# Performance work log

Measured on AMD Instinct MI355X. Metric: run time of the kernel, lower is better.

Reference implementation:

```python
import jax, jax.numpy as jnp
import numpy as np

B = 4
IN_DIM = 512
HID = 1024
MLP_LAYERS = 2
SEQ = 4096          # output_dim / sequence_length
RH = 64             # ripl_hidden_dim
RL = 2              # ripl_num_layers
MULT = 1            # ripl_coordinate_multipler

MID_DIM = 2 * RH * RH + (RH + 1) * RH      # per middle ripple layer param count
OUT_DIM = 2 * RH * 1 + (RH + 1) * 1        # output ripple layer param count
MLP_OUT = RL * MID_DIM + OUT_DIM


def gelu(x):
    return jax.nn.gelu(x, approximate=False)


def layer_norm(x, g, b, eps=1e-5):
    mu = jnp.mean(x, axis=-1, keepdims=True)
    var = jnp.var(x, axis=-1, keepdims=True)
    return (x - mu) * jax.lax.rsqrt(var + eps) * g + b


def batch_ripple(x, w, b):
    # x: (B,S,I), w: (B,O,I,2), b: (B,O,I+1)
    # out[b,s,o] = b[b,o,0] + sum_i b[b,o,i+1] * sin(w[b,o,i,0]*x[b,s,i] + w[b,o,i,1])
    arg = w[:, None, :, :, 0] * x[:, :, None, :] + w[:, None, :, :, 1]  # (B,S,O,I)
    return b[:, None, :, 0] + jnp.sum(jnp.sin(arg) * b[:, None, :, 1:], axis=-1)


def setup_inputs() -> dict:
    key = jax.random.key(0)
    ks = jax.random.split(key, 20)
    s = 0.02
    inp = {
        "x": jax.random.normal(ks[0], (B, IN_DIM), jnp.float32),
        "mlp_w0": jax.random.normal(ks[1], (IN_DIM, HID), jnp.float32) * s,
        "mlp_b0": jnp.zeros((HID,), jnp.float32),
        "mlp_w1": jax.random.normal(ks[2], (HID, HID), jnp.float32) * s,
        "mlp_b1": jnp.zeros((HID,), jnp.float32),
        "ln_g1": jnp.ones((HID,), jnp.float32),
        "ln_b1": jnp.zeros((HID,), jnp.float32),
        "mlp_w2": jax.random.normal(ks[3], (HID, HID), jnp.float32) * s,
        "mlp_b2": jnp.zeros((HID,), jnp.float32),
        "ln_g2": jnp.ones((HID,), jnp.float32),
        "ln_b2": jnp.zeros((HID,), jnp.float32),
        "mlp_w3": jax.random.normal(ks[4], (HID, MLP_OUT), jnp.float32) * s,
        "mlp_b3": jnp.zeros((MLP_OUT,), jnp.float32),
        "lc_w": jax.random.normal(ks[5], (1, RH), jnp.float32) * 0.1,
        "lc_b": jax.random.normal(ks[6], (RH,), jnp.float32) * 0.1,
        "byp_w": jax.random.normal(ks[7], (1, 1, 2), jnp.float32),
        "byp_b": jax.random.normal(ks[8], (1, 2), jnp.float32),
    }
    return inp


def reference(x, mlp_w0, mlp_b0, mlp_w1, mlp_b1, ln_g1, ln_b1,
              mlp_w2, mlp_b2, ln_g2, ln_b2, mlp_w3, mlp_b3,
              lc_w, lc_b, byp_w, byp_b):
    # hypernetwork MLP: Linear+GELU, [Linear+LN+GELU]*2, Linear
    h = gelu(x @ mlp_w0 + mlp_b0)
    h = gelu(layer_norm(h @ mlp_w1 + mlp_b1, ln_g1, ln_b1))
    h = gelu(layer_norm(h @ mlp_w2 + mlp_b2, ln_g2, ln_b2))
    mlp_out = h @ mlp_w3 + mlp_b3                      # (B, MLP_OUT)

    # split into RL middle ripple layers then the output layer
    middles = [mlp_out[:, i * MID_DIM:(i + 1) * MID_DIM] for i in range(RL)]
    out_w = mlp_out[:, RL * MID_DIM:RL * MID_DIM + OUT_DIM]

    # line coordinates -> fc layer
    lc = (jnp.arange(SEQ, dtype=jnp.float32) * MULT)[None, :, None]  # (1,S,1)
    lc = jnp.broadcast_to(lc, (x.shape[0], SEQ, 1))
    lc_x = lc @ lc_w + lc_b                                          # (B,S,RH)
    lc_bypass = lc_x

    for mw in middles:
        w = mw[:, :2 * RH * RH].reshape(-1, RH, RH, 2)
        b = mw[:, 2 * RH * RH:].reshape(-1, RH, RH + 1)
        lc_x = gelu(batch_ripple(lc_x, w, b))

    wo = out_w[:, :2 * RH].reshape(-1, 1, RH, 2)
    bo = out_w[:, 2 * RH:].reshape(-1, 1, RH + 1)
    lc_x = batch_ripple(lc_x, wo, bo)                                # (B,S,1)

    # learned RippleLinear(1,1) bypass, broadcast over features then reduced
    byp = byp_b[0, 0] + jnp.sum(
        jnp.sin(byp_w[0, 0, 0] * lc_bypass + byp_w[0, 0, 1]) * byp_b[0, 1],
        axis=-1, keepdims=True)
    lc_x = lc_x + byp
    return jnp.transpose(lc_x, (0, 2, 1))                            # (B,1,S)
```

## Files before the change

### kernel.cpp

```cpp
#include <hip/hip_runtime.h>
#include <math.h>

#define B_      4
#define IN_DIM  512
#define HID     1024
#define SEQ     4096
#define MID_DIM 12352
#define MLP_OUT 24897
#define INV2PI  0.15915494309189535f

#define MLPT_STRIDE 25088

#define OFF_P0    0
#define OFF_P1    32768
#define OFF_P2    49152
#define OFF_MLPT  65536

__device__ __forceinline__ float gelu_exact(float v) {
    return 0.5f * v * (1.0f + erff(v * 0.70710678118654752f));
}

__device__ __forceinline__ float hw_sin_rev(float r) {
    r = r - __builtin_rintf(r);
    return __builtin_amdgcn_sinf(r);
}

__global__ void k_gemm0(const float* __restrict__ x, const float* __restrict__ w0,
                        float* __restrict__ p0) {
    const int cch = blockIdx.x, kc = blockIdx.y;
    const int tid = threadIdx.x;
    __shared__ float xs[256];
    {
        const int b = tid >> 6, k = tid & 63;
        xs[tid] = x[b * IN_DIM + kc * 64 + k];
    }
    __syncthreads();
    const int b = tid >> 6, cl = tid & 63;
    const int c = cch * 64 + cl;
    const float* wp = w0 + (size_t)(kc * 64) * HID + c;
    const float* xp = xs + b * 64;
    float acc = 0.f;
    #pragma unroll 16
    for (int k = 0; k < 64; ++k) acc = fmaf(xp[k], wp[(size_t)k * HID], acc);
    p0[(kc * 4 + b) * HID + c] = acc;
}

__global__ void k_gemm1(const float* __restrict__ p0, const float* __restrict__ b0,
                        const float* __restrict__ w1, float* __restrict__ p1) {
    const int cch = blockIdx.x, kc = blockIdx.y;
    const int tid = threadIdx.x;
    __shared__ float s_h[1024];
    for (int e = tid; e < 1024; e += 256) {
        const int b = e >> 8, kk = e & 255;
        const int kg = kc * 256 + kk;
        float v = b0[kg];
        #pragma unroll
        for (int j = 0; j < 8; ++j) v += p0[(j * 4 + b) * HID + kg];
        s_h[e] = gelu_exact(v);
    }
    __syncthreads();
    const int b = tid >> 6, cl = tid & 63;
    const int c = cch * 64 + cl;
    const float* wp = w1 + (size_t)(kc * 256) * HID + c;
    const float* hp = s_h + b * 256;
    float acc = 0.f;
    #pragma unroll 16
    for (int k = 0; k < 256; ++k) acc = fmaf(hp[k], wp[(size_t)k * HID], acc);
    p1[(kc * 4 + b) * HID + c] = acc;
}

__global__ void k_gemm2(const float* __restrict__ p1, const float* __restrict__ b1,
                        const float* __restrict__ g1, const float* __restrict__ bl1,
                        const float* __restrict__ w2, float* __restrict__ p2) {
    const int cch = blockIdx.x, kc = blockIdx.y;
    const int tid = threadIdx.x;
    __shared__ __align__(16) float vbuf[4096];
    __shared__ float s_h[1024];
    __shared__ float s_red[8];
    for (int e = tid; e < 4096; e += 256) {
        const int b = e >> 10, c = e & 1023;
        float v = b1[c];
        #pragma unroll
        for (int j = 0; j < 4; ++j) v += p1[(j * 4 + b) * HID + c];
        vbuf[e] = v;
    }
    __syncthreads();
    {
        const int b = tid >> 6, lane = tid & 63;
        float s1 = 0.f, s2 = 0.f;
        #pragma unroll
        for (int jj = 0; jj < 16; ++jj) {
            const float v = vbuf[b * 1024 + lane + 64 * jj];
            s1 += v; s2 += v * v;
        }
        #pragma unroll
        for (int m = 1; m < 64; m <<= 1) {
            s1 += __shfl_xor(s1, m, 64);
            s2 += __shfl_xor(s2, m, 64);
        }
        if (lane == 0) {
            const float mu = s1 * (1.0f / HID);
            s_red[b] = mu;
            s_red[4 + b] = rsqrtf(s2 * (1.0f / HID) - mu * mu + 1e-5f);
        }
    }
    __syncthreads();
    for (int e = tid; e < 1024; e += 256) {
        const int b = e >> 8, kk = e & 255;
        const int c = kc * 256 + kk;
        const float v = vbuf[b * 1024 + c];
        s_h[e] = gelu_exact((v - s_red[b]) * s_red[4 + b] * g1[c] + bl1[c]);
    }
    __syncthreads();
    const int b = tid >> 6, cl = tid & 63;
    const int c = cch * 64 + cl;
    const float* wp = w2 + (size_t)(kc * 256) * HID + c;
    const float* hp = s_h + b * 256;
    float acc = 0.f;
    #pragma unroll 16
    for (int k = 0; k < 256; ++k) acc = fmaf(hp[k], wp[(size_t)k * HID], acc);
    p2[(kc * 4 + b) * HID + c] = acc;
}

__global__ void k_gemm3T(const float* __restrict__ p2, const float* __restrict__ b2,
                         const float* __restrict__ g2, const float* __restrict__ bl2,
                         const float* __restrict__ w3, const float* __restrict__ b3,
                         float* __restrict__ mlpT) {
    const int colb = blockIdx.x;
    const int kc   = blockIdx.y;
    const int tid  = threadIdx.x;
    __shared__ __align__(16) float vbuf[4096];
    __shared__ __align__(16) float s_h[512];
    __shared__ float s_red[8];

    for (int e = tid; e < 4096; e += 256) {
        const int b = e >> 10, c = e & 1023;
        float v = b2[c];
        #pragma unroll
        for (int j = 0; j < 4; ++j) v += p2[(j * 4 + b) * HID + c];
        vbuf[e] = v;
    }
    __syncthreads();
    {
        const int b = tid >> 6, lane = tid & 63;
        float s1 = 0.f, s2 = 0.f;
        #pragma unroll
        for (int jj = 0; jj < 16; ++jj) {
            const float v = vbuf[b * 1024 + lane + 64 * jj];
            s1 += v; s2 += v * v;
        }
        #pragma unroll
        for (int m = 1; m < 64; m <<= 1) {
            s1 += __shfl_xor(s1, m, 64);
            s2 += __shfl_xor(s2, m, 64);
        }
        if (lane == 0) {
            const float mu = s1 * (1.0f / HID);
            s_red[b] = mu;
            s_red[4 + b] = rsqrtf(s2 * (1.0f / HID) - mu * mu + 1e-5f);
        }
    }
    __syncthreads();
    for (int e = tid; e < 512; e += 256) {
        const int b = e >> 7, kk = e & 127;
        const int c = kc * 128 + kk;
        const float v = vbuf[b * 1024 + c];
        s_h[e] = gelu_exact((v - s_red[b]) * s_red[4 + b] * g2[c] + bl2[c]);
    }
    __syncthreads();

    const int c_raw = colb * 256 + tid;
    const bool valid = c_raw < MLP_OUT;
    const int c = valid ? c_raw : (MLP_OUT - 1);
    const float* wp = w3 + (size_t)(kc * 128) * MLP_OUT + c;
    float a0 = 0.f, a1 = 0.f, a2 = 0.f, a3 = 0.f;
    #pragma unroll 8
    for (int kk = 0; kk < 128; kk += 4) {
        const float wv0 = wp[(size_t)(kk + 0) * MLP_OUT];
        const float wv1 = wp[(size_t)(kk + 1) * MLP_OUT];
        const float wv2 = wp[(size_t)(kk + 2) * MLP_OUT];
        const float wv3 = wp[(size_t)(kk + 3) * MLP_OUT];
        const float4 h0 = *reinterpret_cast<const float4*>(&s_h[kk]);
        const float4 h1 = *reinterpret_cast<const float4*>(&s_h[128 + kk]);
        const float4 h2 = *reinterpret_cast<const float4*>(&s_h[256 + kk]);
        const float4 h3 = *reinterpret_cast<const float4*>(&s_h[384 + kk]);
        a0 = fmaf(h0.x, wv0, fmaf(h0.y, wv1, fmaf(h0.z, wv2, fmaf(h0.w, wv3, a0))));
        a1 = fmaf(h1.x, wv0, fmaf(h1.y, wv1, fmaf(h1.z, wv2, fmaf(h1.w, wv3, a1))));
        a2 = fmaf(h2.x, wv0, fmaf(h2.y, wv1, fmaf(h2.z, wv2, fmaf(h2.w, wv3, a2))));
        a3 = fmaf(h3.x, wv0, fmaf(h3.y, wv1, fmaf(h3.z, wv2, fmaf(h3.w, wv3, a3))));
    }
    if (!valid) return;

    int d; float sc = 1.f;
    if (c < 2 * MID_DIM) {
        const int l = c / MID_DIM;
        const int rel = c - l * MID_DIM;
        if (rel < 8192) {
            const int o = rel >> 7, low = rel & 127;
            d = l * 12416 + (low & 1) * 4096 + (low >> 1) * 64 + o;
            sc = INV2PI;
        } else {
            const int r2 = rel - 8192;
            const int o = r2 / 65, j = r2 % 65;
            d = (j == 0) ? (l * 12416 + 12288 + o)
                         : (l * 12416 + 8192 + (j - 1) * 64 + o);
        }
    } else {
        const int rel = c - 2 * MID_DIM;
        if (rel < 128)       { d = 24832 + (rel & 1) * 64 + (rel >> 1); sc = INV2PI; }
        else if (rel == 128) { d = 24832 + 192; }
        else                 { d = 24832 + 128 + (rel - 129); }
    }
    const float bias = (kc == 0) ? b3[c] : 0.f;
    atomicAdd(&mlpT[(size_t)0 * MLPT_STRIDE + d], (a0 + bias) * sc);
    atomicAdd(&mlpT[(size_t)1 * MLPT_STRIDE + d], (a1 + bias) * sc);
    atomicAdd(&mlpT[(size_t)2 * MLPT_STRIDE + d], (a2 + bias) * sc);
    atomicAdd(&mlpT[(size_t)3 * MLPT_STRIDE + d], (a3 + bias) * sc);
}

__global__ void __launch_bounds__(256, 2) k_ripple(
        const float* __restrict__ mlpT, const float* __restrict__ lcw,
        const float* __restrict__ lcb, const float* __restrict__ bypw,
        const float* __restrict__ bypb, float* __restrict__ out) {
    const int tid = threadIdx.x;
    const int b = blockIdx.y;
    const int t0 = blockIdx.x * 32;
    const int lane = tid & 63, wid = tid >> 6, tb = wid * 8;

    __shared__ __align__(16) float s_w[12416];
    __shared__ __align__(16) float s_x[2304];
    __shared__ __align__(16) float s_wo[256];
    __shared__ float s_red[32];

    const float* mb = mlpT + (size_t)b * MLPT_STRIDE;

    {
        const float4* src = reinterpret_cast<const float4*>(mb);
        float4* dst = reinterpret_cast<float4*>(s_w);
        for (int e = tid; e < 3104; e += 256) dst[e] = src[e];
        if (tid < 64)
            reinterpret_cast<float4*>(s_wo)[tid] =
                reinterpret_cast<const float4*>(mb + 24832)[tid];
    }
    const float lw = lcw[lane], lb = lcb[lane];
    for (int e = tid; e < 2048; e += 256) {
        const int i = e >> 5, tt = e & 31;
        s_x[i * 36 + tt] = fmaf((float)(t0 + tt), lcw[i], lcb[i]);
    }
    __syncthreads();

    float acc[8];
    for (int layer = 0; layer < 2; ++layer) {
        const float bc = s_w[12288 + lane];
        #pragma unroll
        for (int j = 0; j < 8; ++j) acc[j] = bc;
        for (int i = 0; i < 64; ++i) {
            const float wsv = s_w[i * 64 + lane];
            const float wov = s_w[4096 + i * 64 + lane];
            const float bsv = s_w[8192 + i * 64 + lane];
            const float4 xa = *reinterpret_cast<const float4*>(&s_x[i * 36 + tb]);
            const float4 xb = *reinterpret_cast<const float4*>(&s_x[i * 36 + tb + 4]);
            const float xv[8] = {xa.x, xa.y, xa.z, xa.w, xb.x, xb.y, xb.z, xb.w};
            #pragma unroll
            for (int j = 0; j < 8; ++j) {
                const float r = fmaf(wsv, xv[j], wov);
                acc[j] = fmaf(hw_sin_rev(r), bsv, acc[j]);
            }
        }
        __syncthreads();
        if (layer == 0) {
            #pragma unroll
            for (int j = 0; j < 8; ++j)
                s_x[lane * 36 + tb + j] = gelu_exact(acc[j]);
            const float4* src = reinterpret_cast<const float4*>(mb + 12416);
            float4* dst = reinterpret_cast<float4*>(s_w);
            for (int e = tid; e < 3104; e += 256) dst[e] = src[e];
            __syncthreads();
        }
    }

    {
        const float wsO = s_wo[lane], woO = s_wo[64 + lane], bsO = s_wo[128 + lane];
        const float bcO = s_wo[192];
        const float bw0 = bypw[0] * INV2PI, bw1 = bypw[1] * INV2PI;
        const float bb0 = bypb[0], bb1 = bypb[1];
        #pragma unroll
        for (int j = 0; j < 8; ++j) {
            const int t = t0 + tb + j;
            const float v = gelu_exact(acc[j]);
            float s = hw_sin_rev(fmaf(wsO, v, woO)) * bsO;
            const float xb = fmaf((float)t, lw, lb);
            s = fmaf(hw_sin_rev(fmaf(bw0, xb, bw1)), bb1, s);
            #pragma unroll
            for (int m = 1; m < 64; m <<= 1) s += __shfl_xor(s, m, 64);
            if (lane == 0) s_red[tb + j] = s + bcO + bb0;
        }
    }
    __syncthreads();
    if (tid < 32) out[(size_t)b * SEQ + t0 + tid] = s_red[tid];
}

extern "C" void kernel_launch(void* const* d_in, const int* in_sizes, int n_in,
                              void* d_out, int out_size, void* d_ws, size_t ws_size,
                              hipStream_t stream) {
    const float* x    = (const float*)d_in[0];
    const float* w0   = (const float*)d_in[1];
    const float* b0   = (const float*)d_in[2];
    const float* w1   = (const float*)d_in[3];
    const float* b1   = (const float*)d_in[4];
    const float* g1   = (const float*)d_in[5];
    const float* bl1  = (const float*)d_in[6];
    const float* w2   = (const float*)d_in[7];
    const float* b2   = (const float*)d_in[8];
    const float* g2   = (const float*)d_in[9];
    const float* bl2  = (const float*)d_in[10];
    const float* w3   = (const float*)d_in[11];
    const float* b3   = (const float*)d_in[12];
    const float* lcw  = (const float*)d_in[13];
    const float* lcb  = (const float*)d_in[14];
    const float* bypw = (const float*)d_in[15];
    const float* bypb = (const float*)d_in[16];
    float* out = (float*)d_out;
    float* ws  = (float*)d_ws;

    float* p0   = ws + OFF_P0;
    float* p1   = ws + OFF_P1;
    float* p2   = ws + OFF_P2;
    float* mlpT = ws + OFF_MLPT;

    k_gemm0 <<<dim3(16, 8), 256, 0, stream>>>(x, w0, p0);
    k_gemm1 <<<dim3(16, 4), 256, 0, stream>>>(p0, b0, w1, p1);
    k_gemm2 <<<dim3(16, 4), 256, 0, stream>>>(p1, b1, g1, bl1, w2, p2);
    hipMemsetAsync(mlpT, 0, (size_t)B_ * MLPT_STRIDE * sizeof(float), stream);
    k_gemm3T<<<dim3(98, 8), 256, 0, stream>>>(p2, b2, g2, bl2, w3, b3, mlpT);
    k_ripple<<<dim3(SEQ / 32, B_), 256, 0, stream>>>(mlpT, lcw, lcb, bypw, bypb, out);
}
```

Baseline: 310.1 us.

## Replace gemm3 atomics with partial buffer plus combine kernel, split K finer

The last MLP GEMM now writes per-K-chunk partial sums to a workspace buffer, and a new combine kernel reduces them, adds the bias and scatters into the transposed parameter layout. This replaces the memset and the atomicAdd scatter. The weight loads in gemm3 are software-pipelined with a 16-deep register double buffer, and gemm1/gemm2 double their K-split to run more blocks. The sine wrapper uses a fract builtin when available. In exchange it adds one kernel launch and extra partial-sum traffic through global memory.

```diff
diff --git a/kernel.cpp b/kernel.cpp
--- a/kernel.cpp
+++ b/kernel.cpp
@@ -13,16 +13,21 @@
 
 #define OFF_P0    0
 #define OFF_P1    32768
-#define OFF_P2    49152
-#define OFF_MLPT  65536
+#define OFF_P2    65536
+#define OFF_P3    98304
+#define OFF_MLPT  895008
 
 __device__ __forceinline__ float gelu_exact(float v) {
     return 0.5f * v * (1.0f + erff(v * 0.70710678118654752f));
 }
 
 __device__ __forceinline__ float hw_sin_rev(float r) {
+#if __has_builtin(__builtin_amdgcn_fractf)
+    return __builtin_amdgcn_sinf(__builtin_amdgcn_fractf(r));
+#else
     r = r - __builtin_rintf(r);
     return __builtin_amdgcn_sinf(r);
+#endif
 }
 
 __global__ void k_gemm0(const float* __restrict__ x, const float* __restrict__ w0,
@@ -49,10 +54,10 @@
                         const float* __restrict__ w1, float* __restrict__ p1) {
     const int cch = blockIdx.x, kc = blockIdx.y;
     const int tid = threadIdx.x;
-    __shared__ float s_h[1024];
-    for (int e = tid; e < 1024; e += 256) {
-        const int b = e >> 8, kk = e & 255;
-        const int kg = kc * 256 + kk;
+    __shared__ float s_h[512];
+    for (int e = tid; e < 512; e += 256) {
+        const int b = e >> 7, kk = e & 127;
+        const int kg = kc * 128 + kk;
         float v = b0[kg];
         #pragma unroll
         for (int j = 0; j < 8; ++j) v += p0[(j * 4 + b) * HID + kg];
@@ -61,11 +66,11 @@
     __syncthreads();
     const int b = tid >> 6, cl = tid & 63;
     const int c = cch * 64 + cl;
-    const float* wp = w1 + (size_t)(kc * 256) * HID + c;
-    const float* hp = s_h + b * 256;
+    const float* wp = w1 + (size_t)(kc * 128) * HID + c;
+    const float* hp = s_h + b * 128;
     float acc = 0.f;
     #pragma unroll 16
-    for (int k = 0; k < 256; ++k) acc = fmaf(hp[k], wp[(size_t)k * HID], acc);
+    for (int k = 0; k < 128; ++k) acc = fmaf(hp[k], wp[(size_t)k * HID], acc);
     p1[(kc * 4 + b) * HID + c] = acc;
 }
 
@@ -75,13 +80,13 @@
     const int cch = blockIdx.x, kc = blockIdx.y;
     const int tid = threadIdx.x;
     __shared__ __align__(16) float vbuf[4096];
-    __shared__ float s_h[1024];
+    __shared__ float s_h[512];
     __shared__ float s_red[8];
     for (int e = tid; e < 4096; e += 256) {
         const int b = e >> 10, c = e & 1023;
         float v = b1[c];
         #pragma unroll
-        for (int j = 0; j < 4; ++j) v += p1[(j * 4 + b) * HID + c];
+        for (int j = 0; j < 8; ++j) v += p1[(j * 4 + b) * HID + c];
         vbuf[e] = v;
     }
     __syncthreads();
@@ -105,39 +110,38 @@
         }
     }
     __syncthreads();
-    for (int e = tid; e < 1024; e += 256) {
-        const int b = e >> 8, kk = e & 255;
-        const int c = kc * 256 + kk;
+    for (int e = tid; e < 512; e += 256) {
+        const int b = e >> 7, kk = e & 127;
+        const int c = kc * 128 + kk;
         const float v = vbuf[b * 1024 + c];
         s_h[e] = gelu_exact((v - s_red[b]) * s_red[4 + b] * g1[c] + bl1[c]);
     }
     __syncthreads();
     const int b = tid >> 6, cl = tid & 63;
     const int c = cch * 64 + cl;
-    const float* wp = w2 + (size_t)(kc * 256) * HID + c;
-    const float* hp = s_h + b * 256;
+    const float* wp = w2 + (size_t)(kc * 128) * HID + c;
+    const float* hp = s_h + b * 128;
     float acc = 0.f;
     #pragma unroll 16
-    for (int k = 0; k < 256; ++k) acc = fmaf(hp[k], wp[(size_t)k * HID], acc);
+    for (int k = 0; k < 128; ++k) acc = fmaf(hp[k], wp[(size_t)k * HID], acc);
     p2[(kc * 4 + b) * HID + c] = acc;
 }
 
-__global__ void k_gemm3T(const float* __restrict__ p2, const float* __restrict__ b2,
-                         const float* __restrict__ g2, const float* __restrict__ bl2,
-                         const float* __restrict__ w3, const float* __restrict__ b3,
-                         float* __restrict__ mlpT) {
+__global__ void k_gemm3(const float* __restrict__ p2, const float* __restrict__ b2,
+                        const float* __restrict__ g2, const float* __restrict__ bl2,
+                        const float* __restrict__ w3, float* __restrict__ p3) {
     const int colb = blockIdx.x;
     const int kc   = blockIdx.y;
     const int tid  = threadIdx.x;
     __shared__ __align__(16) float vbuf[4096];
-    __shared__ __align__(16) float s_h[512];
+    __shared__ float s_h[512];
     __shared__ float s_red[8];
 
     for (int e = tid; e < 4096; e += 256) {
         const int b = e >> 10, c = e & 1023;
         float v = b2[c];
         #pragma unroll
-        for (int j = 0; j < 4; ++j) v += p2[(j * 4 + b) * HID + c];
+        for (int j = 0; j < 8; ++j) v += p2[(j * 4 + b) * HID + c];
         vbuf[e] = v;
     }
     __syncthreads();
@@ -173,24 +177,51 @@
     const bool valid = c_raw < MLP_OUT;
     const int c = valid ? c_raw : (MLP_OUT - 1);
     const float* wp = w3 + (size_t)(kc * 128) * MLP_OUT + c;
+
     float a0 = 0.f, a1 = 0.f, a2 = 0.f, a3 = 0.f;
-    #pragma unroll 8
-    for (int kk = 0; kk < 128; kk += 4) {
-        const float wv0 = wp[(size_t)(kk + 0) * MLP_OUT];
-        const float wv1 = wp[(size_t)(kk + 1) * MLP_OUT];
-        const float wv2 = wp[(size_t)(kk + 2) * MLP_OUT];
-        const float wv3 = wp[(size_t)(kk + 3) * MLP_OUT];
-        const float4 h0 = *reinterpret_cast<const float4*>(&s_h[kk]);
-        const float4 h1 = *reinterpret_cast<const float4*>(&s_h[128 + kk]);
-        const float4 h2 = *reinterpret_cast<const float4*>(&s_h[256 + kk]);
-        const float4 h3 = *reinterpret_cast<const float4*>(&s_h[384 + kk]);
-        a0 = fmaf(h0.x, wv0, fmaf(h0.y, wv1, fmaf(h0.z, wv2, fmaf(h0.w, wv3, a0))));
-        a1 = fmaf(h1.x, wv0, fmaf(h1.y, wv1, fmaf(h1.z, wv2, fmaf(h1.w, wv3, a1))));
-        a2 = fmaf(h2.x, wv0, fmaf(h2.y, wv1, fmaf(h2.z, wv2, fmaf(h2.w, wv3, a2))));
-        a3 = fmaf(h3.x, wv0, fmaf(h3.y, wv1, fmaf(h3.z, wv2, fmaf(h3.w, wv3, a3))));
+    float wb[16];
+    #pragma unroll
+    for (int j = 0; j < 16; ++j) wb[j] = wp[(size_t)j * MLP_OUT];
+
+    for (int g = 0; g < 7; ++g) {
+        const int k0 = g * 16;
+        float wn[16];
+        #pragma unroll
+        for (int j = 0; j < 16; ++j) wn[j] = wp[(size_t)(k0 + 16 + j) * MLP_OUT];
+        #pragma unroll
+        for (int j = 0; j < 16; ++j) {
+            const int k = k0 + j;
+            a0 = fmaf(s_h[k],       wb[j], a0);
+            a1 = fmaf(s_h[128 + k], wb[j], a1);
+            a2 = fmaf(s_h[256 + k], wb[j], a2);
+            a3 = fmaf(s_h[384 + k], wb[j], a3);
+        }
+        #pragma unroll
+        for (int j = 0; j < 16; ++j) wb[j] = wn[j];
+    }
+    #pragma unroll
+    for (int j = 0; j < 16; ++j) {
+        const int k = 112 + j;
+        a0 = fmaf(s_h[k],       wb[j], a0);
+        a1 = fmaf(s_h[128 + k], wb[j], a1);
+        a2 = fmaf(s_h[256 + k], wb[j], a2);
+        a3 = fmaf(s_h[384 + k], wb[j], a3);
     }
     if (!valid) return;
-
+    p3[(size_t)(kc * 4 + 0) * MLP_OUT + c] = a0;
+    p3[(size_t)(kc * 4 + 1) * MLP_OUT + c] = a1;
+    p3[(size_t)(kc * 4 + 2) * MLP_OUT + c] = a2;
+    p3[(size_t)(kc * 4 + 3) * MLP_OUT + c] = a3;
+}
+
+__global__ void k_comb3T(const float* __restrict__ p3, const float* __restrict__ b3,
+                         float* __restrict__ mlpT) {
+    const int b = blockIdx.y;
+    const int c = blockIdx.x * 256 + threadIdx.x;
+    if (c >= MLP_OUT) return;
+    float v = b3[c];
+    #pragma unroll
+    for (int j = 0; j < 8; ++j) v += p3[(size_t)(j * 4 + b) * MLP_OUT + c];
     int d; float sc = 1.f;
     if (c < 2 * MID_DIM) {
         const int l = c / MID_DIM;
@@ -211,11 +242,7 @@
         else if (rel == 128) { d = 24832 + 192; }
         else                 { d = 24832 + 128 + (rel - 129); }
     }
-    const float bias = (kc == 0) ? b3[c] : 0.f;
-    atomicAdd(&mlpT[(size_t)0 * MLPT_STRIDE + d], (a0 + bias) * sc);
-    atomicAdd(&mlpT[(size_t)1 * MLPT_STRIDE + d], (a1 + bias) * sc);
-    atomicAdd(&mlpT[(size_t)2 * MLPT_STRIDE + d], (a2 + bias) * sc);
-    atomicAdd(&mlpT[(size_t)3 * MLPT_STRIDE + d], (a3 + bias) * sc);
+    mlpT[(size_t)b * MLPT_STRIDE + d] = v * sc;
 }
 
 __global__ void __launch_bounds__(256, 2) k_ripple(
@@ -326,12 +353,13 @@
     float* p0   = ws + OFF_P0;
     float* p1   = ws + OFF_P1;
     float* p2   = ws + OFF_P2;
+    float* p3   = ws + OFF_P3;
     float* mlpT = ws + OFF_MLPT;
 
     k_gemm0 <<<dim3(16, 8), 256, 0, stream>>>(x, w0, p0);
-    k_gemm1 <<<dim3(16, 4), 256, 0, stream>>>(p0, b0, w1, p1);
-    k_gemm2 <<<dim3(16, 4), 256, 0, stream>>>(p1, b1, g1, bl1, w2, p2);
-    hipMemsetAsync(mlpT, 0, (size_t)B_ * MLPT_STRIDE * sizeof(float), stream);
-    k_gemm3T<<<dim3(98, 8), 256, 0, stream>>>(p2, b2, g2, bl2, w3, b3, mlpT);
+    k_gemm1 <<<dim3(16, 8), 256, 0, stream>>>(p0, b0, w1, p1);
+    k_gemm2 <<<dim3(16, 8), 256, 0, stream>>>(p1, b1, g1, bl1, w2, p2);
+    k_gemm3 <<<dim3(98, 8), 256, 0, stream>>>(p2, b2, g2, bl2, w3, p3);
+    k_comb3T<<<dim3(98, 4), 256, 0, stream>>>(p3, b3, mlpT);
     k_ripple<<<dim3(SEQ / 32, B_), 256, 0, stream>>>(mlpT, lcw, lcb, bypw, bypb, out);
 }
```

New measurement: 305.3 us. About the same (-1.5%).
